# Performance work log

Hardware: AMD Instinct MI355X
Metric: run time of the kernel (lower is better)

## Reference

```python
import jax, jax.numpy as jnp
import numpy as np

N_NODES = 50000
N_EDGES = 800000
F_IN = 64
HID = 128
N_GRAPHS = 64
F_OUT = 1
NEG_SLOPE = 0.2


def _glorot(key, shape):
    fan_in, fan_out = shape[0], shape[-1]
    s = jnp.sqrt(6.0 / (fan_in + fan_out))
    return jax.random.uniform(key, shape, jnp.float32, -s, s)


def setup_inputs() -> dict:
    key = jax.random.key(0)
    ks = jax.random.split(key, 24)
    inp = {
        "x": jax.random.normal(ks[0], (N_NODES, F_IN), jnp.float32),
        "edge_index": jax.random.randint(ks[1], (2, N_EDGES), 0, N_NODES, jnp.int32),
        "edge_weight": jax.random.uniform(ks[2], (N_EDGES, 1), jnp.float32),
        "batch": jnp.sort(jax.random.randint(ks[3], (N_NODES,), 0, N_GRAPHS, jnp.int32)),
        # GATv2Conv layer 1 (heads=1): lin_l, lin_r (with bias), lin_edge (no bias), att, out-bias
        "W1l": _glorot(ks[4], (F_IN, HID)), "b1l": jnp.zeros((HID,), jnp.float32),
        "W1r": _glorot(ks[5], (F_IN, HID)), "b1r": jnp.zeros((HID,), jnp.float32),
        "We1": _glorot(ks[6], (1, HID)),
        "att1": _glorot(ks[7], (HID, 1))[:, 0],
        "bias1": jnp.zeros((HID,), jnp.float32),
        # GATv2Conv layer 2
        "W2l": _glorot(ks[8], (HID, HID)), "b2l": jnp.zeros((HID,), jnp.float32),
        "W2r": _glorot(ks[9], (HID, HID)), "b2r": jnp.zeros((HID,), jnp.float32),
        "We2": _glorot(ks[10], (1, HID)),
        "att2": _glorot(ks[11], (HID, 1))[:, 0],
        "bias2": jnp.zeros((HID,), jnp.float32),
        # final Linear
        "Wlin": _glorot(ks[12], (HID, F_OUT)),
        "blin": jnp.zeros((F_OUT,), jnp.float32),
    }
    return inp


def gatv2_layer(x, src, dst, eattr, Wl, bl, Wr, br, We, att, bias):
    n = x.shape[0]
    # add_self_loops=True with edge_attr fill_value='mean'
    loop = jnp.arange(n, dtype=src.dtype)
    src = jnp.concatenate([src, loop])
    dst = jnp.concatenate([dst, loop])
    mean_attr = jnp.mean(eattr, axis=0, keepdims=True)  # [1, edge_dim]
    eattr = jnp.concatenate([eattr, jnp.broadcast_to(mean_attr, (n, eattr.shape[1]))])
    xl = x @ Wl + bl            # [N, HID] source transform
    xr = x @ Wr + br            # [N, HID] dest transform
    ee = eattr @ We             # [E', HID] edge embedding
    m = jax.nn.leaky_relu(xl[src] + xr[dst] + ee, NEG_SLOPE)  # [E', HID]
    logits = m @ att            # [E']
    # per-destination softmax (every node has a self loop, so no empty segments)
    lmax = jax.ops.segment_max(logits, dst, num_segments=n)
    w = jnp.exp(logits - lmax[dst])
    denom = jax.ops.segment_sum(w, dst, num_segments=n)
    alpha = w / denom[dst]
    out = jax.ops.segment_sum(xl[src] * alpha[:, None], dst, num_segments=n)
    return out + bias


def reference(x, edge_index, edge_weight, batch,
              W1l, b1l, W1r, b1r, We1, att1, bias1,
              W2l, b2l, W2r, b2r, We2, att2, bias2,
              Wlin, blin):
    src, dst = edge_index[0], edge_index[1]
    h = jax.nn.relu(gatv2_layer(x, src, dst, edge_weight, W1l, b1l, W1r, b1r, We1, att1, bias1))
    h = jax.nn.relu(gatv2_layer(h, src, dst, edge_weight, W2l, b2l, W2r, b2r, We2, att2, bias2))
    # global_mean_pool over graph assignment
    sums = jax.ops.segment_sum(h, batch, num_segments=N_GRAPHS)
    cnt = jax.ops.segment_sum(jnp.ones((h.shape[0],), h.dtype), batch, num_segments=N_GRAPHS)
    pooled = sums / jnp.maximum(cnt, 1.0)[:, None]
    return pooled @ Wlin + blin  # [N_GRAPHS, F_OUT]
```

## Files before the change

kernel.cpp:

```cpp
#include <hip/hip_runtime.h>

#define NN 50000
#define NE 800000
#define EP (NE + NN)
#define HID 128
#define FIN 64
#define NG 64
#define SLOPE 0.2f

typedef unsigned short ushort_t;
typedef unsigned int uint_t;

__device__ __forceinline__ float wred_sum(float v) {
  for (int off = 32; off; off >>= 1) v += __shfl_xor(v, off);
  return v;
}
__device__ __forceinline__ ushort_t f2bf(float f) {
  uint_t b = __float_as_uint(f);
  b += 0x7fffu + ((b >> 16) & 1u);
  return (ushort_t)(b >> 16);
}

#define FMA4(A_, S_, W_) \
  A_.x += (S_) * W_.x; A_.y += (S_) * W_.y; \
  A_.z += (S_) * W_.z; A_.w += (S_) * W_.w;

__global__ void k_mean(const float* __restrict__ ew, float* __restrict__ meansum) {
  int tid = blockIdx.x * blockDim.x + threadIdx.x;
  int stride = gridDim.x * blockDim.x;
  float s = 0.f;
  for (int i = tid; i < NE; i += stride) s += ew[i];
  s = wred_sum(s);
  if ((threadIdx.x & 63) == 0) atomicAdd(meansum, s);
}

__global__ void k_hist(const int* __restrict__ edst, int* __restrict__ counts) {
  int tid = blockIdx.x * blockDim.x + threadIdx.x;
  int stride = gridDim.x * blockDim.x;
  for (int i = tid; i < EP; i += stride) {
    int d = (i < NE) ? edst[i] : (i - NE);
    atomicAdd(&counts[d], 1);
  }
}

__global__ void k_scan(int* __restrict__ counts, int* __restrict__ starts) {
  __shared__ int wsum[16];
  __shared__ int woff[16];
  int t = threadIdx.x;
  int lane = t & 63;
  int w = t >> 6;
  int carry = 0;
  for (int base = 0; base < NN; base += 1024) {
    int i = base + t;
    int v = (i < NN) ? counts[i] : 0;
    if (i < NN) counts[i] = 0;
    int sc = v;
    #pragma unroll
    for (int d = 1; d < 64; d <<= 1) {
      int u = __shfl_up(sc, d);
      if (lane >= d) sc += u;
    }
    if (lane == 63) wsum[w] = sc;
    __syncthreads();
    if (w == 0 && lane < 16) {
      int x = wsum[lane];
      #pragma unroll
      for (int d = 1; d < 16; d <<= 1) {
        int u = __shfl_up(x, d);
        if (lane >= d) x += u;
      }
      woff[lane] = x;
    }
    __syncthreads();
    int waveoff = (w == 0) ? 0 : woff[w - 1];
    if (i < NN) starts[i] = carry + waveoff + sc - v;
    carry += woff[15];
    __syncthreads();
  }
  if (t == 0) starts[NN] = carry;
}

__global__ void k_scatter(const int* __restrict__ esrc, const int* __restrict__ edst,
                          const float* __restrict__ ew, const float* __restrict__ meansum,
                          const int* __restrict__ starts, int* __restrict__ cursor,
                          int2* __restrict__ emeta) {
  float mw = meansum[0] * (1.0f / NE);
  int tid = blockIdx.x * blockDim.x + threadIdx.x;
  int stride = gridDim.x * blockDim.x;
  for (int i = tid; i < EP; i += stride) {
    int s, d; float wv;
    if (i < NE) { s = esrc[i]; d = edst[i]; wv = ew[i]; }
    else        { s = d = i - NE; wv = mw; }
    int pos = starts[d] + atomicAdd(&cursor[d], 1);
    emeta[pos] = make_int2(s, __float_as_int(wv));
  }
}

template <int K>
__global__ __launch_bounds__(256) void k_gemm2(const float* __restrict__ A,
                                               const float* __restrict__ Wl,
                                               const float* __restrict__ bl,
                                               const float* __restrict__ Wr,
                                               const float* __restrict__ br,
                                               ushort_t* __restrict__ xlout,
                                               float* __restrict__ xrout, int n) {
  __shared__ float As[64][K];
  int t = threadIdx.x;
  int nb = blockIdx.x * 64;
  constexpr int F4 = 16 * K;
  for (int i = t; i < F4; i += 256) {
    int row = i / (K / 4);
    int c = (i % (K / 4)) * 4;
    int gn = nb + row;
    float4 v = make_float4(0.f, 0.f, 0.f, 0.f);
    if (gn < n) v = *(const float4*)(A + (size_t)gn * K + c);
    *(float4*)&As[row][c] = v;
  }
  __syncthreads();
  int fx = (t & 31) * 4;
  int ny = (t >> 5) * 8;
  float4 accL[8], accR[8];
  #pragma unroll
  for (int j = 0; j < 8; ++j) {
    accL[j] = make_float4(0.f, 0.f, 0.f, 0.f);
    accR[j] = make_float4(0.f, 0.f, 0.f, 0.f);
  }
  for (int k4 = 0; k4 < K; k4 += 4) {
    float4 wl0 = *(const float4*)(Wl + (size_t)(k4 + 0) * HID + fx);
    float4 wl1 = *(const float4*)(Wl + (size_t)(k4 + 1) * HID + fx);
    float4 wl2 = *(const float4*)(Wl + (size_t)(k4 + 2) * HID + fx);
    float4 wl3 = *(const float4*)(Wl + (size_t)(k4 + 3) * HID + fx);
    float4 wr0 = *(const float4*)(Wr + (size_t)(k4 + 0) * HID + fx);
    float4 wr1 = *(const float4*)(Wr + (size_t)(k4 + 1) * HID + fx);
    float4 wr2 = *(const float4*)(Wr + (size_t)(k4 + 2) * HID + fx);
    float4 wr3 = *(const float4*)(Wr + (size_t)(k4 + 3) * HID + fx);
    #pragma unroll
    for (int j = 0; j < 8; ++j) {
      float4 a = *(const float4*)&As[ny + j][k4];
      FMA4(accL[j], a.x, wl0); FMA4(accL[j], a.y, wl1);
      FMA4(accL[j], a.z, wl2); FMA4(accL[j], a.w, wl3);
      FMA4(accR[j], a.x, wr0); FMA4(accR[j], a.y, wr1);
      FMA4(accR[j], a.z, wr2); FMA4(accR[j], a.w, wr3);
    }
  }
  float4 bbl = *(const float4*)(bl + fx);
  float4 bbr = *(const float4*)(br + fx);
  #pragma unroll
  for (int j = 0; j < 8; ++j) {
    int gn = nb + ny + j;
    if (gn < n) {
      ushort4 u4;
      u4.x = f2bf(accL[j].x + bbl.x); u4.y = f2bf(accL[j].y + bbl.y);
      u4.z = f2bf(accL[j].z + bbl.z); u4.w = f2bf(accL[j].w + bbl.w);
      *(ushort4*)(xlout + (size_t)gn * HID + fx) = u4;
      float4 o = make_float4(accR[j].x + bbr.x, accR[j].y + bbr.y,
                             accR[j].z + bbr.z, accR[j].w + bbr.w);
      *(float4*)(xrout + (size_t)gn * HID + fx) = o;
    }
  }
}

__global__ __launch_bounds__(256, 4) void k_fused(const ushort_t* __restrict__ xl16,
                                                  const float* __restrict__ xr,
                                                  const int2* __restrict__ emeta,
                                                  const int* __restrict__ starts,
                                                  const float* __restrict__ We,
                                                  const float* __restrict__ att,
                                                  const float* __restrict__ bias,
                                                  float* __restrict__ hout) {
  int node = blockIdx.x * (blockDim.x >> 6) + (threadIdx.x >> 6);
  int lane = threadIdx.x & 63;
  if (node >= NN) return;
  int hl = lane & 31;
  int half = lane >> 5;
  int s0 = starts[node], s1 = starts[node + 1];
  int f = hl * 4;
  float4 xro = *(const float4*)(xr + (size_t)node * HID + f);
  float4 we  = *(const float4*)(We + f);
  float4 at  = *(const float4*)(att + f);

  int emy = 8 * half + ((hl >> 2) & 7);
  bool b4 = (hl & 16) != 0;
  bool b3 = (hl & 8) != 0;
  bool b2 = (hl & 4) != 0;

  float ssum = 0.f;
  float4 acc = make_float4(0.f, 0.f, 0.f, 0.f);

  for (int i0 = s0; i0 < s1; i0 += 16) {
    int base = i0 + 8 * half;
    uint2 g[8];
    float p[8];
    #pragma unroll
    for (int k = 0; k < 8; ++k) {
      int idx = min(base + k, s1 - 1);
      int2 em = emeta[idx];
      p[k] = __int_as_float(em.y);
      g[k] = *(const uint2*)(xl16 + (size_t)em.x * HID + f);
    }
    #pragma unroll
    for (int k = 0; k < 8; ++k) {
      float wk = p[k];
      float t0 = __uint_as_float(g[k].x << 16)          + xro.x + wk * we.x;
      float t1 = __uint_as_float(g[k].x & 0xffff0000u)  + xro.y + wk * we.y;
      float t2 = __uint_as_float(g[k].y << 16)          + xro.z + wk * we.z;
      float t3 = __uint_as_float(g[k].y & 0xffff0000u)  + xro.w + wk * we.w;
      t0 = t0 > 0.f ? t0 : SLOPE * t0;
      t1 = t1 > 0.f ? t1 : SLOPE * t1;
      t2 = t2 > 0.f ? t2 : SLOPE * t2;
      t3 = t3 > 0.f ? t3 : SLOPE * t3;
      p[k] = t0 * at.x + t1 * at.y + t2 * at.z + t3 * at.w;
    }
    float sdv, rcv;
    float q0, q1, q2, q3;
    sdv = b4 ? p[0] : p[4]; rcv = __shfl_xor(sdv, 16, 32); q0 = (b4 ? p[4] : p[0]) + rcv;
    sdv = b4 ? p[1] : p[5]; rcv = __shfl_xor(sdv, 16, 32); q1 = (b4 ? p[5] : p[1]) + rcv;
    sdv = b4 ? p[2] : p[6]; rcv = __shfl_xor(sdv, 16, 32); q2 = (b4 ? p[6] : p[2]) + rcv;
    sdv = b4 ? p[3] : p[7]; rcv = __shfl_xor(sdv, 16, 32); q3 = (b4 ? p[7] : p[3]) + rcv;
    float r0, r1;
    sdv = b3 ? q0 : q2; rcv = __shfl_xor(sdv, 8, 32); r0 = (b3 ? q2 : q0) + rcv;
    sdv = b3 ? q1 : q3; rcv = __shfl_xor(sdv, 8, 32); r1 = (b3 ? q3 : q1) + rcv;
    sdv = b2 ? r0 : r1; rcv = __shfl_xor(sdv, 4, 32);
    float lg = (b2 ? r1 : r0) + rcv;
    lg += __shfl_xor(lg, 1, 32);
    lg += __shfl_xor(lg, 2, 32);
    float w = (i0 + emy < s1) ? __expf(lg) : 0.f;
    ssum += w;
    #pragma unroll
    for (int k = 0; k < 8; ++k) {
      float wk = __shfl(w, k << 2, 32);
      acc.x += wk * __uint_as_float(g[k].x << 16);
      acc.y += wk * __uint_as_float(g[k].x & 0xffff0000u);
      acc.z += wk * __uint_as_float(g[k].y << 16);
      acc.w += wk * __uint_as_float(g[k].y & 0xffff0000u);
    }
  }
  acc.x += __shfl_xor(acc.x, 32);
  acc.y += __shfl_xor(acc.y, 32);
  acc.z += __shfl_xor(acc.z, 32);
  acc.w += __shfl_xor(acc.w, 32);
  float st = wred_sum(ssum) * 0.25f;
  float inv = 1.0f / st;
  if (half == 0) {
    float4 bb = *(const float4*)(bias + f);
    float4 o;
    o.x = fmaxf(acc.x * inv + bb.x, 0.f);
    o.y = fmaxf(acc.y * inv + bb.y, 0.f);
    o.z = fmaxf(acc.z * inv + bb.z, 0.f);
    o.w = fmaxf(acc.w * inv + bb.w, 0.f);
    *(float4*)(hout + (size_t)node * HID + f) = o;
  }
}

__global__ void k_bounds(const int* __restrict__ batch, int* __restrict__ gs) {
  int i = blockIdx.x * blockDim.x + threadIdx.x;
  if (i >= NN) return;
  int b = batch[i];
  if (i == 0) {
    for (int g = 0; g <= b; ++g) gs[g] = 0;
  }
  int bn = (i + 1 < NN) ? batch[i + 1] : NG;
  for (int g = b + 1; g <= bn; ++g) gs[g] = i + 1;
}

__global__ __launch_bounds__(256) void k_pool(const float* __restrict__ h,
                                              const int* __restrict__ gs,
                                              const float* __restrict__ Wlin,
                                              const float* __restrict__ blin,
                                              float* __restrict__ out) {
  __shared__ float red[256];
  int g = blockIdx.x;
  int t = threadIdx.x;
  int f = t & 127;
  int half = t >> 7;
  int n0 = gs[g], n1 = gs[g + 1];
  float s0 = 0.f, s1 = 0.f, s2 = 0.f, s3 = 0.f;
  int n = n0 + half;
  for (; n + 6 < n1; n += 8) {
    s0 += h[(size_t)n * HID + f];
    s1 += h[(size_t)(n + 2) * HID + f];
    s2 += h[(size_t)(n + 4) * HID + f];
    s3 += h[(size_t)(n + 6) * HID + f];
  }
  for (; n < n1; n += 2) s0 += h[(size_t)n * HID + f];
  red[t] = (s0 + s1) + (s2 + s3);
  __syncthreads();
  if (t < 128) {
    float pooled = red[t] + red[t + 128];
    float cnt = (float)max(n1 - n0, 1);
    red[t] = (pooled / cnt) * Wlin[f];
  }
  __syncthreads();
  if (t < 64) {
    float v = red[t] + red[t + 64];
    v = wred_sum(v);
    if (t == 0) out[g] = v + blin[0];
  }
}

extern "C" void kernel_launch(void* const* d_in, const int* in_sizes, int n_in,
                              void* d_out, int out_size, void* d_ws, size_t ws_size,
                              hipStream_t stream) {
  const float* x     = (const float*)d_in[0];
  const int*   ei    = (const int*)d_in[1];
  const float* ew    = (const float*)d_in[2];
  const int*   batch = (const int*)d_in[3];
  const float* W1l = (const float*)d_in[4];
  const float* b1l = (const float*)d_in[5];
  const float* W1r = (const float*)d_in[6];
  const float* b1r = (const float*)d_in[7];
  const float* We1 = (const float*)d_in[8];
  const float* at1 = (const float*)d_in[9];
  const float* bi1 = (const float*)d_in[10];
  const float* W2l = (const float*)d_in[11];
  const float* b2l = (const float*)d_in[12];
  const float* W2r = (const float*)d_in[13];
  const float* b2r = (const float*)d_in[14];
  const float* We2 = (const float*)d_in[15];
  const float* at2 = (const float*)d_in[16];
  const float* bi2 = (const float*)d_in[17];
  const float* Wlin = (const float*)d_in[18];
  const float* blin = (const float*)d_in[19];

  float* ws = (float*)d_ws;
  size_t o = 0;
  float*    xr    = ws + o; o += (size_t)NN * HID;
  float*    hb    = ws + o; o += (size_t)NN * HID;
  ushort_t* xl16  = (ushort_t*)(ws + o); o += (size_t)NN * HID / 2;
  int2*     emeta = (int2*)(ws + o); o += (size_t)2 * EP;
  int*      starts = (int*)(ws + o); o += NN + 1;
  int*      gs     = (int*)(ws + o); o += NG + 1;
  size_t zoff = o;
  int*      counts  = (int*)(ws + o); o += NN;
  float*    meansum = ws + o; o += 1;
  size_t zero_bytes = (o - zoff) * sizeof(float);

  hipMemsetAsync(counts, 0, zero_bytes, stream);

  k_mean<<<256, 256, 0, stream>>>(ew, meansum);
  k_hist<<<1024, 256, 0, stream>>>(ei + NE, counts);
  k_scan<<<1, 1024, 0, stream>>>(counts, starts);
  k_scatter<<<1024, 256, 0, stream>>>(ei, ei + NE, ew, meansum, starts, counts,
                                      emeta);
  k_bounds<<<(NN + 255) / 256, 256, 0, stream>>>(batch, gs);

  int gb  = (NN + 63) / 64;
  int nbn = (NN + 3) / 4;

  k_gemm2<FIN><<<gb, 256, 0, stream>>>(x, W1l, b1l, W1r, b1r, xl16, xr, NN);
  k_fused<<<nbn, 256, 0, stream>>>(xl16, xr, emeta, starts, We1, at1, bi1, hb);
  k_gemm2<HID><<<gb, 256, 0, stream>>>(hb, W2l, b2l, W2r, b2r, xl16, xr, NN);
  k_fused<<<nbn, 256, 0, stream>>>(xl16, xr, emeta, starts, We2, at2, bi2, hb);
  k_pool<<<NG, 256, 0, stream>>>(hb, gs, Wlin, blin, (float*)d_out);
}
```

Measured before the change: 421.8 us.

## Parallelize CSR prefix scan across blocks and fuse histogram with mean reduction

Replaces the single-block serial scan over 50000 counts with a three-phase multi-block scan (per-block scan, block-sum scan, add offsets). Merges the edge-weight mean reduction into the histogram kernel, and accounts for self-loops analytically (+1 per node) instead of atomics. This targets the latency of a one-block scan loop and removes a launch, at the cost of two extra small kernel launches.

```diff
diff --git a/kernel.cpp b/kernel.cpp
--- a/kernel.cpp
+++ b/kernel.cpp
@@ -7,6 +7,7 @@
 #define FIN 64
 #define NG 64
 #define SLOPE 0.2f
+#define NB 49
 
 typedef unsigned short ushort_t;
 typedef unsigned int uint_t;
@@ -25,59 +26,71 @@
   A_.x += (S_) * W_.x; A_.y += (S_) * W_.y; \
   A_.z += (S_) * W_.z; A_.w += (S_) * W_.w;
 
-__global__ void k_mean(const float* __restrict__ ew, float* __restrict__ meansum) {
+__global__ void k_hist2(const int* __restrict__ edst, const float* __restrict__ ew,
+                        int* __restrict__ counts, float* __restrict__ meansum) {
   int tid = blockIdx.x * blockDim.x + threadIdx.x;
   int stride = gridDim.x * blockDim.x;
   float s = 0.f;
-  for (int i = tid; i < NE; i += stride) s += ew[i];
+  for (int i = tid; i < NE; i += stride) {
+    atomicAdd(&counts[edst[i]], 1);
+    s += ew[i];
+  }
   s = wred_sum(s);
   if ((threadIdx.x & 63) == 0) atomicAdd(meansum, s);
 }
 
-__global__ void k_hist(const int* __restrict__ edst, int* __restrict__ counts) {
-  int tid = blockIdx.x * blockDim.x + threadIdx.x;
-  int stride = gridDim.x * blockDim.x;
-  for (int i = tid; i < EP; i += stride) {
-    int d = (i < NE) ? edst[i] : (i - NE);
-    atomicAdd(&counts[d], 1);
-  }
-}
-
-__global__ void k_scan(int* __restrict__ counts, int* __restrict__ starts) {
+__global__ __launch_bounds__(1024) void k_scan1(const int* __restrict__ counts,
+                                                int* __restrict__ starts,
+                                                int* __restrict__ bsum) {
   __shared__ int wsum[16];
   __shared__ int woff[16];
+  int t = threadIdx.x, lane = t & 63, w = t >> 6;
+  int i = blockIdx.x * 1024 + t;
+  int v = (i < NN) ? counts[i] + 1 : 0;
+  int sc = v;
+  #pragma unroll
+  for (int d = 1; d < 64; d <<= 1) {
+    int u = __shfl_up(sc, d);
+    if (lane >= d) sc += u;
+  }
+  if (lane == 63) wsum[w] = sc;
+  __syncthreads();
+  if (w == 0 && lane < 16) {
+    int x = wsum[lane];
+    #pragma unroll
+    for (int d = 1; d < 16; d <<= 1) {
+      int u = __shfl_up(x, d);
+      if (lane >= d) x += u;
+    }
+    woff[lane] = x;
+  }
+  __syncthreads();
+  int waveoff = (w == 0) ? 0 : woff[w - 1];
+  if (i < NN) starts[i] = waveoff + sc - v;
+  if (t == 1023) bsum[blockIdx.x] = woff[15];
+}
+
+__global__ void k_scan2(int* __restrict__ bsum, int* __restrict__ starts) {
   int t = threadIdx.x;
-  int lane = t & 63;
-  int w = t >> 6;
-  int carry = 0;
-  for (int base = 0; base < NN; base += 1024) {
-    int i = base + t;
-    int v = (i < NN) ? counts[i] : 0;
-    if (i < NN) counts[i] = 0;
-    int sc = v;
-    #pragma unroll
-    for (int d = 1; d < 64; d <<= 1) {
-      int u = __shfl_up(sc, d);
-      if (lane >= d) sc += u;
-    }
-    if (lane == 63) wsum[w] = sc;
-    __syncthreads();
-    if (w == 0 && lane < 16) {
-      int x = wsum[lane];
-      #pragma unroll
-      for (int d = 1; d < 16; d <<= 1) {
-        int u = __shfl_up(x, d);
-        if (lane >= d) x += u;
-      }
-      woff[lane] = x;
-    }
-    __syncthreads();
-    int waveoff = (w == 0) ? 0 : woff[w - 1];
-    if (i < NN) starts[i] = carry + waveoff + sc - v;
-    carry += woff[15];
-    __syncthreads();
-  }
-  if (t == 0) starts[NN] = carry;
+  int v = (t < NB) ? bsum[t] : 0;
+  int sc = v;
+  #pragma unroll
+  for (int d = 1; d < 64; d <<= 1) {
+    int u = __shfl_up(sc, d);
+    if (t >= d) sc += u;
+  }
+  if (t < NB) bsum[t] = sc - v;
+  if (t == 0) starts[NN] = EP;
+}
+
+__global__ __launch_bounds__(1024) void k_scan3(int* __restrict__ starts,
+                                                const int* __restrict__ bsum,
+                                                int* __restrict__ counts) {
+  int i = blockIdx.x * 1024 + threadIdx.x;
+  if (i < NN) {
+    starts[i] += bsum[blockIdx.x];
+    counts[i] = 0;
+  }
 }
 
 __global__ void k_scatter(const int* __restrict__ esrc, const int* __restrict__ edst,
@@ -330,6 +343,7 @@
   int2*     emeta = (int2*)(ws + o); o += (size_t)2 * EP;
   int*      starts = (int*)(ws + o); o += NN + 1;
   int*      gs     = (int*)(ws + o); o += NG + 1;
+  int*      bsum   = (int*)(ws + o); o += NB;
   size_t zoff = o;
   int*      counts  = (int*)(ws + o); o += NN;
   float*    meansum = ws + o; o += 1;
@@ -337,9 +351,10 @@
 
   hipMemsetAsync(counts, 0, zero_bytes, stream);
 
-  k_mean<<<256, 256, 0, stream>>>(ew, meansum);
-  k_hist<<<1024, 256, 0, stream>>>(ei + NE, counts);
-  k_scan<<<1, 1024, 0, stream>>>(counts, starts);
+  k_hist2<<<1024, 256, 0, stream>>>(ei + NE, ew, counts, meansum);
+  k_scan1<<<NB, 1024, 0, stream>>>(counts, starts, bsum);
+  k_scan2<<<1, 64, 0, stream>>>(bsum, starts);
+  k_scan3<<<NB, 1024, 0, stream>>>(starts, bsum, counts);
   k_scatter<<<1024, 256, 0, stream>>>(ei, ei + NE, ew, meansum, starts, counts,
                                       emeta);
   k_bounds<<<(NN + 255) / 256, 256, 0, stream>>>(batch, gs);
```

New measurement: 405.6 us. -3.8%, faster.
